# Optimization experiments

Measured on AMD Instinct MI355X. Metric: run time of the kernel, lower is better.

The kernel has to match this reference:

```python
import jax, jax.numpy as jnp
import numpy as np

B, NQ, D, NH, DH = 16, 300, 256, 8, 32
L, P, FFN = 3, 4, 1024
LEVEL_SHAPES = [(80, 80), (40, 40), (20, 20)]
S = sum(h * w for h, w in LEVEL_SHAPES)  # 8400
EPS = 1e-5

PARAM_NAMES = ['wq', 'bq', 'wk', 'bk', 'wv', 'bv', 'wo', 'bo', 'ln1_g', 'ln1_b',
               'w_off', 'b_off', 'w_aw', 'b_aw', 'w_val', 'b_val', 'w_out', 'b_out',
               'ln2_g', 'ln2_b', 'w_fc1', 'b_fc1', 'w_fc2', 'b_fc2', 'ln3_g', 'ln3_b']


def _ln(x, g, b):
    m = jnp.mean(x, -1, keepdims=True)
    v = jnp.mean(jnp.square(x - m), -1, keepdims=True)
    return (x - m) * jax.lax.rsqrt(v + EPS) * g + b


def _bilinear(v_l, loc, Hl, Wl):
    # v_l: [B, Hl*Wl, NH, DH]; loc in [0,1]: [B, NQ, NH, P, 2]
    # matches torch grid_sample(align_corners=False, padding='zeros') with grid=2*loc-1
    x = loc[..., 0] * Wl - 0.5
    y = loc[..., 1] * Hl - 0.5
    x0 = jnp.floor(x)
    y0 = jnp.floor(y)
    vt = v_l.transpose(0, 2, 1, 3)  # [B, NH, Sl, DH]
    out = jnp.zeros((v_l.shape[0], NQ, NH, P, DH), v_l.dtype)
    for dx in (0, 1):
        for dy in (0, 1):
            xi = x0 + dx
            yi = y0 + dy
            w = (1.0 - jnp.abs(x - xi)) * (1.0 - jnp.abs(y - yi))
            valid = (xi >= 0) & (xi < Wl) & (yi >= 0) & (yi < Hl)
            idx = (jnp.clip(yi, 0, Hl - 1) * Wl + jnp.clip(xi, 0, Wl - 1)).astype(jnp.int32)
            idx_t = idx.transpose(0, 2, 1, 3).reshape(idx.shape[0], NH, NQ * P)
            g = jnp.take_along_axis(vt, idx_t[..., None], axis=2)  # [B, NH, NQ*P, DH]
            g = g.reshape(-1, NH, NQ, P, DH).transpose(0, 2, 1, 3, 4)
            out = out + g * (w * valid)[..., None]
    return out  # [B, NQ, NH, P, DH]


def _forward(hidden_states, pos_embed, encoder_hidden_states, reference_points, spatial_shapes, p):
    h = hidden_states
    # ---- self-attention (pos added to q and k only) ----
    hp = h + pos_embed
    q = (hp @ p['wq'] + p['bq']).reshape(B, NQ, NH, DH)
    k = (hp @ p['wk'] + p['bk']).reshape(B, NQ, NH, DH)
    v = (h @ p['wv'] + p['bv']).reshape(B, NQ, NH, DH)
    scores = jnp.einsum('bqhd,bkhd->bhqk', q, k) * (1.0 / np.sqrt(DH).astype(np.float32))
    attn = jax.nn.softmax(scores, -1)
    sa = jnp.einsum('bhqk,bkhd->bqhd', attn, v).reshape(B, NQ, D) @ p['wo'] + p['bo']
    h = _ln(h + sa, p['ln1_g'], p['ln1_b'])

    # ---- multiscale deformable cross-attention ----
    hp = h + pos_embed
    value = (encoder_hidden_states @ p['w_val'] + p['b_val']).reshape(B, S, NH, DH)
    off = (hp @ p['w_off'] + p['b_off']).reshape(B, NQ, NH, L, P, 2)
    aw = jax.nn.softmax((hp @ p['w_aw'] + p['b_aw']).reshape(B, NQ, NH, L * P), -1)
    aw = aw.reshape(B, NQ, NH, L, P)
    normalizer = jnp.stack([spatial_shapes[:, 1], spatial_shapes[:, 0]], -1).astype(h.dtype)  # [L,2] = (W,H)
    loc = reference_points[:, :, None, :, None, :] + off / normalizer[None, None, None, :, None, :]
    out = jnp.zeros((B, NQ, NH, DH), h.dtype)
    start = 0
    for l, (Hl, Wl) in enumerate(LEVEL_SHAPES):
        v_l = value[:, start:start + Hl * Wl]
        sampled = _bilinear(v_l, loc[:, :, :, l], Hl, Wl)  # [B,NQ,NH,P,DH]
        out = out + jnp.sum(sampled * aw[:, :, :, l, :, None], axis=3)
        start += Hl * Wl
    ca = out.reshape(B, NQ, D) @ p['w_out'] + p['b_out']
    h = _ln(h + ca, p['ln2_g'], p['ln2_b'])

    # ---- MLP ----
    mlp = jax.nn.relu(h @ p['w_fc1'] + p['b_fc1']) @ p['w_fc2'] + p['b_fc2']
    return _ln(h + mlp, p['ln3_g'], p['ln3_b'])


def setup_inputs() -> dict:
    key = jax.random.key(0)
    ks = iter(jax.random.split(key, 48))
    def nrm(shape, s=0.02):
        return jax.random.normal(next(ks), shape, jnp.float32) * s
    inp = {
        'hidden_states': jax.random.normal(next(ks), (B, NQ, D), jnp.float32),
        'pos_embed': jax.random.normal(next(ks), (B, NQ, D), jnp.float32),
        'encoder_hidden_states': jax.random.normal(next(ks), (B, S, D), jnp.float32),
        'reference_points': jax.random.uniform(next(ks), (B, NQ, L, 2), jnp.float32),
        'spatial_shapes': jnp.array(LEVEL_SHAPES, jnp.int32),
        'wq': nrm((D, D)), 'bq': jnp.zeros(D),
        'wk': nrm((D, D)), 'bk': jnp.zeros(D),
        'wv': nrm((D, D)), 'bv': jnp.zeros(D),
        'wo': nrm((D, D)), 'bo': jnp.zeros(D),
        'ln1_g': jnp.ones(D), 'ln1_b': jnp.zeros(D),
        'w_off': nrm((D, NH * L * P * 2)), 'b_off': nrm((NH * L * P * 2,), 0.1),
        'w_aw': nrm((D, NH * L * P)), 'b_aw': jnp.zeros(NH * L * P),
        'w_val': nrm((D, D)), 'b_val': jnp.zeros(D),
        'w_out': nrm((D, D)), 'b_out': jnp.zeros(D),
        'ln2_g': jnp.ones(D), 'ln2_b': jnp.zeros(D),
        'w_fc1': nrm((D, FFN)), 'b_fc1': jnp.zeros(FFN),
        'w_fc2': nrm((FFN, D)), 'b_fc2': jnp.zeros(D),
        'ln3_g': jnp.ones(D), 'ln3_b': jnp.zeros(D),
    }
    return inp


def reference(hidden_states, pos_embed, encoder_hidden_states, reference_points, spatial_shapes,
              wq, bq, wk, bk, wv, bv, wo, bo, ln1_g, ln1_b,
              w_off, b_off, w_aw, b_aw, w_val, b_val, w_out, b_out,
              ln2_g, ln2_b, w_fc1, b_fc1, w_fc2, b_fc2, ln3_g, ln3_b):
    p = dict(wq=wq, bq=bq, wk=wk, bk=bk, wv=wv, bv=bv, wo=wo, bo=bo,
             ln1_g=ln1_g, ln1_b=ln1_b, w_off=w_off, b_off=b_off, w_aw=w_aw, b_aw=b_aw,
             w_val=w_val, b_val=b_val, w_out=w_out, b_out=b_out, ln2_g=ln2_g, ln2_b=ln2_b,
             w_fc1=w_fc1, b_fc1=b_fc1, w_fc2=w_fc2, b_fc2=b_fc2, ln3_g=ln3_g, ln3_b=ln3_b)
    return _forward(hidden_states, pos_embed, encoder_hidden_states, reference_points, spatial_shapes, p)
```

## Files before the change

### kernel.cpp

```cpp
#include <hip/hip_runtime.h>
#include <hip/hip_bf16.h>
#include <math.h>

#define B_   16
#define NQ_  300
#define D_   256
#define NH_  8
#define DH_  32
#define L_   3
#define P_   4
#define FFN_ 1024
#define S_   8400
#define ROWS_ (B_*NQ_)
#define NB_   (ROWS_*D_)

typedef __attribute__((ext_vector_type(4))) unsigned short ushort4_t;
typedef __attribute__((ext_vector_type(8))) unsigned short ushort8_t;
typedef __attribute__((ext_vector_type(8))) short bf16x8;
typedef __attribute__((ext_vector_type(4))) float f32x4;

__device__ inline unsigned short f2b(float f) {
    __hip_bfloat16 h = __float2bfloat16(f);
    return __builtin_bit_cast(unsigned short, h);
}
__device__ inline float b2f(unsigned short u) {
    union { unsigned u; float f; } c; c.u = ((unsigned)u) << 16; return c.f;
}

__global__ __launch_bounds__(256) void prep_kernel(
    const float* __restrict__ wq, const float* __restrict__ wk,
    const float* __restrict__ wv, const float* __restrict__ wo,
    const float* __restrict__ w_val, const float* __restrict__ w_out,
    const float* __restrict__ w_off, const float* __restrict__ w_aw,
    const float* __restrict__ w_fc1, const float* __restrict__ w_fc2,
    const float* __restrict__ bq, const float* __restrict__ bk,
    const float* __restrict__ b_off, const float* __restrict__ b_aw,
    unsigned short* __restrict__ wtqk, unsigned short* __restrict__ wtv,
    unsigned short* __restrict__ wto, unsigned short* __restrict__ wtval,
    unsigned short* __restrict__ wtout, unsigned short* __restrict__ wtoa,
    unsigned short* __restrict__ wtfc1, unsigned short* __restrict__ wtfc2,
    float* __restrict__ bqk, float* __restrict__ boa)
{
    const int bid = blockIdx.x;
    if (bid >= 968) {
        int idx = (bid - 968)*256 + threadIdx.x;
        if (idx < 512) bqk[idx] = (idx < 256) ? bq[idx] : bk[idx-256];
        else { int j = idx - 512; if (j < 288) boa[j] = (j < 192) ? b_off[j] : b_aw[j-192]; }
        return;
    }
    const float* src; unsigned short* dst; int K, N, t;
    if      (bid < 64)  { src=wq;    dst=wtqk;         K=256;  N=256;  t=bid; }
    else if (bid < 128) { src=wk;    dst=wtqk+65536;   K=256;  N=256;  t=bid-64; }
    else if (bid < 192) { src=wv;    dst=wtv;          K=256;  N=256;  t=bid-128; }
    else if (bid < 256) { src=wo;    dst=wto;          K=256;  N=256;  t=bid-192; }
    else if (bid < 320) { src=w_val; dst=wtval;        K=256;  N=256;  t=bid-256; }
    else if (bid < 384) { src=w_out; dst=wtout;        K=256;  N=256;  t=bid-320; }
    else if (bid < 432) { src=w_off; dst=wtoa;         K=256;  N=192;  t=bid-384; }
    else if (bid < 456) { src=w_aw;  dst=wtoa+49152;   K=256;  N=96;   t=bid-432; }
    else if (bid < 712) { src=w_fc1; dst=wtfc1;        K=256;  N=1024; t=bid-456; }
    else                { src=w_fc2; dst=wtfc2;        K=1024; N=256;  t=bid-712; }

    __shared__ unsigned short tl[32][33];
    int tid = threadIdx.x;
    int tx = tid & 31, ty = tid >> 5;
    int ntx = N >> 5;
    int n0 = (t % ntx) * 32, k0 = (t / ntx) * 32;
    #pragma unroll
    for (int i = 0; i < 4; ++i)
        tl[tx][ty + i*8] = f2b(src[(size_t)(k0 + ty + i*8)*N + n0 + tx]);
    __syncthreads();
    #pragma unroll
    for (int i = 0; i < 4; ++i)
        dst[(size_t)(n0 + ty + i*8)*K + k0 + tx] = tl[ty + i*8][tx];
}

#define GEMM_PREAMBLE()                                                        \
    const int tid  = threadIdx.x;                                              \
    const int lane = tid & 63;                                                 \
    const int w    = tid >> 6;                                                 \
    const int wr   = w >> 1, wc = w & 1;                                       \
    const int m0   = blockIdx.y * 64;                                          \
    const int n0   = blockIdx.x * 128;                                         \
    const int fr   = lane & 15, fq = lane >> 4;                                \
    const int arow = tid >> 2, aseg = (tid & 3) * 8;                           \
    const int brow = tid >> 1, bseg = (tid & 1) * 16;                          \
    const bool a_ok = (m0 + arow) < M;                                         \
    const bool b_ok = (n0 + brow) < N;                                         \
    const float*          aptr  = A  + (size_t)(m0 + arow)*K + aseg;           \
    const float*          aptr2 = A2 ? A2 + (size_t)(m0 + arow)*K + aseg : (const float*)0; \
    const unsigned short* bptr  = WT + (size_t)(n0 + brow)*K + bseg;           \
    f32x4 acc[2][4];                                                           \
    _Pragma("unroll") for (int m = 0; m < 2; ++m)                              \
        _Pragma("unroll") for (int n = 0; n < 4; ++n)                          \
            acc[m][n] = (f32x4){0.f, 0.f, 0.f, 0.f};                           \
    float4 avA0, avB0, avA1, avB1;                                             \
    ushort8_t bvA0, bvB0, bvA1, bvB1;

#define GEMM_LOAD(avA, avB, bvA, bvB, kk) do {                                 \
    if (a_ok) {                                                                \
        avA = *(const float4*)(aptr + (kk));                                   \
        avB = *(const float4*)(aptr + (kk) + 4);                               \
        if (aptr2) {                                                           \
            float4 x2 = *(const float4*)(aptr2 + (kk));                        \
            float4 y2 = *(const float4*)(aptr2 + (kk) + 4);                    \
            avA.x += x2.x; avA.y += x2.y; avA.z += x2.z; avA.w += x2.w;        \
            avB.x += y2.x; avB.y += y2.y; avB.z += y2.z; avB.w += y2.w;        \
        }                                                                      \
    } else { avA = (float4){0,0,0,0}; avB = (float4){0,0,0,0}; }               \
    if (b_ok) { bvA = *(const ushort8_t*)(bptr + (kk));                        \
                bvB = *(const ushort8_t*)(bptr + (kk) + 8); }                  \
    else { _Pragma("unroll") for (int j = 0; j < 8; ++j){bvA[j]=0;bvB[j]=0;} } \
} while (0)

#define GEMM_STORE_LDS(avA, avB, bvA, bvB) do {                                \
    ushort8_t ac;                                                              \
    ac[0]=f2b(avA.x); ac[1]=f2b(avA.y); ac[2]=f2b(avA.z); ac[3]=f2b(avA.w);    \
    ac[4]=f2b(avB.x); ac[5]=f2b(avB.y); ac[6]=f2b(avB.z); ac[7]=f2b(avB.w);    \
    *(ushort8_t*)&As[arow][aseg]     = ac;                                     \
    *(ushort8_t*)&Bs[brow][bseg]     = bvA;                                    \
    *(ushort8_t*)&Bs[brow][bseg + 8] = bvB;                                    \
} while (0)

#define GEMM_COMPUTE() do {                                                    \
    bf16x8 af[2], bfv[4];                                                      \
    _Pragma("unroll") for (int m = 0; m < 2; ++m)                              \
        af[m] = *(const bf16x8*)&As[wr*32 + m*16 + fr][fq*8];                  \
    _Pragma("unroll") for (int n = 0; n < 4; ++n)                              \
        bfv[n] = *(const bf16x8*)&Bs[wc*64 + n*16 + fr][fq*8];                 \
    _Pragma("unroll") for (int m = 0; m < 2; ++m)                              \
        _Pragma("unroll") for (int n = 0; n < 4; ++n)                          \
            acc[m][n] = __builtin_amdgcn_mfma_f32_16x16x32_bf16(               \
                af[m], bfv[n], acc[m][n], 0, 0, 0);                            \
} while (0)

#define GEMM_KLOOP()                                                           \
    GEMM_LOAD(avA0, avB0, bvA0, bvB0, 0);                                      \
    for (int k0 = 0; k0 < K; k0 += 64) {                                       \
        __syncthreads();                                                       \
        GEMM_STORE_LDS(avA0, avB0, bvA0, bvB0);                                \
        GEMM_LOAD(avA1, avB1, bvA1, bvB1, k0 + 32);                            \
        __syncthreads();                                                       \
        GEMM_COMPUTE();                                                        \
        __syncthreads();                                                       \
        GEMM_STORE_LDS(avA1, avB1, bvA1, bvB1);                                \
        if (k0 + 64 < K) GEMM_LOAD(avA0, avB0, bvA0, bvB0, k0 + 64);           \
        __syncthreads();                                                       \
        GEMM_COMPUTE();                                                        \
    }

__global__ __launch_bounds__(256) void gemm_mfma64(
    const float* __restrict__ A, const float* __restrict__ A2,
    const unsigned short* __restrict__ WT,
    const float* __restrict__ bias, float* __restrict__ C,
    int M, int N, int K, int relu)
{
    __shared__ unsigned short As[64][40];
    __shared__ unsigned short Bs[128][40];
    GEMM_PREAMBLE();
    GEMM_KLOOP();

    #pragma unroll
    for (int n = 0; n < 4; ++n) {
        int col = n0 + wc*64 + n*16 + fr;
        if (col < N) {
            float bcol = bias[col];
            #pragma unroll
            for (int m = 0; m < 2; ++m) {
                int rbase = m0 + wr*32 + m*16 + fq*4;
                #pragma unroll
                for (int r = 0; r < 4; ++r) {
                    int row = rbase + r;
                    if (row < M) {
                        float vv = acc[m][n][r] + bcol;
                        if (relu) vv = fmaxf(vv, 0.f);
                        C[(size_t)row * N + col] = vv;
                    }
                }
            }
        }
    }
}

__global__ __launch_bounds__(256) void stage1_kernel(
    const float* __restrict__ ehs, const float* __restrict__ h_in,
    const float* __restrict__ pos,
    const unsigned short* __restrict__ wtval, const float* __restrict__ b_val,
    unsigned short* __restrict__ val_bf,
    const unsigned short* __restrict__ wtqk, const float* __restrict__ bqk,
    float* __restrict__ buf_qk,
    const unsigned short* __restrict__ wtv, const float* __restrict__ bv,
    float* __restrict__ buf_v)
{
    __shared__ unsigned short As[64][40];
    __shared__ unsigned short Bs[128][40];

    const int bid = blockIdx.x;
    int path, m0, n0, Ncols = 256;
    const float* Ap; const float* A2p = nullptr;
    const unsigned short* Bp; const float* bias; float* C = nullptr;
    if (bid < 4200) {
        path = 0; m0 = (bid >> 1)*64; n0 = (bid & 1)*128;
        Ap = ehs; Bp = wtval; bias = b_val;
    } else if (bid < 4500) {
        int t = bid - 4200;
        path = 1; m0 = (t >> 2)*64; n0 = (t & 3)*128;
        Ap = h_in; A2p = pos; Bp = wtqk; bias = bqk; C = buf_qk; Ncols = 512;
    } else {
        int t = bid - 4500;
        path = 2; m0 = (t >> 1)*64; n0 = (t & 1)*128;
        Ap = h_in; Bp = wtv; bias = bv; C = buf_v;
    }

    const int tid  = threadIdx.x;
    const int lane = tid & 63;
    const int w    = tid >> 6;
    const int wr   = w >> 1, wc = w & 1;
    const int fr   = lane & 15, fq = lane >> 4;
    const int arow = tid >> 2, aseg = (tid & 3) * 8;
    const int brow = tid >> 1, bseg = (tid & 1) * 16;
    const bool a_ok = true, b_ok = true;
    const int K = 256;
    const float*          aptr  = Ap + (size_t)(m0 + arow)*256 + aseg;
    const float*          aptr2 = A2p ? A2p + (size_t)(m0 + arow)*256 + aseg : (const float*)0;
    const unsigned short* bptr  = Bp + (size_t)(n0 + brow)*256 + bseg;

    f32x4 acc[2][4];
    #pragma unroll
    for (int m = 0; m < 2; ++m)
        #pragma unroll
        for (int n = 0; n < 4; ++n)
            acc[m][n] = (f32x4){0.f, 0.f, 0.f, 0.f};
    float4 avA0, avB0, avA1, avB1;
    ushort8_t bvA0, bvB0, bvA1, bvB1;

    GEMM_KLOOP();

    if (path == 0) {
        #pragma unroll
        for (int n = 0; n < 4; ++n) {
            int col = n0 + wc*64 + n*16 + fr;
            int hh = col >> 5, dd = col & 31;
            float bcol = bias[col];
            #pragma unroll
            for (int m = 0; m < 2; ++m) {
                int rbase = m0 + wr*32 + m*16 + fq*4;
                #pragma unroll
                for (int r = 0; r < 4; ++r) {
                    unsigned row = rbase + r;
                    unsigned bb = row / (unsigned)S_;
                    unsigned ss = row - bb * (unsigned)S_;
                    val_bf[((size_t)(bb*NH_ + hh)*S_ + ss)*DH_ + dd] = f2b(acc[m][n][r] + bcol);
                }
            }
        }
    } else {
        #pragma unroll
        for (int n = 0; n < 4; ++n) {
            int col = n0 + wc*64 + n*16 + fr;
            float bcol = bias[col];
            #pragma unroll
            for (int m = 0; m < 2; ++m) {
                int rbase = m0 + wr*32 + m*16 + fq*4;
                #pragma unroll
                for (int r = 0; r < 4; ++r)
                    C[(size_t)(rbase + r) * Ncols + col] = acc[m][n][r] + bcol;
            }
        }
    }
}

__global__ __launch_bounds__(256) void gemm_relu_bf16(
    const float* __restrict__ A, const unsigned short* __restrict__ WT,
    const float* __restrict__ bias, unsigned short* __restrict__ OUT,
    int M, int N, int K)
{
    __shared__ unsigned short As[64][40];
    __shared__ unsigned short Bs[128][40];
    const float* A2 = nullptr;
    GEMM_PREAMBLE();
    GEMM_KLOOP();

    #pragma unroll
    for (int n = 0; n < 4; ++n) {
        int col = n0 + wc*64 + n*16 + fr;
        float bcol = bias[col];
        #pragma unroll
        for (int m = 0; m < 2; ++m) {
            int rbase = m0 + wr*32 + m*16 + fq*4;
            #pragma unroll
            for (int r = 0; r < 4; ++r)
                OUT[(size_t)(rbase + r) * N + col] = f2b(fmaxf(acc[m][n][r] + bcol, 0.f));
        }
    }
}

__global__ __launch_bounds__(256) void gemm_bfA(
    const unsigned short* __restrict__ A, const unsigned short* __restrict__ WT,
    const float* __restrict__ bias, float* __restrict__ C,
    int M, int N, int K)
{
    __shared__ unsigned short As[64][40];
    __shared__ unsigned short Bs[128][40];

    const int tid  = threadIdx.x;
    const int lane = tid & 63;
    const int w    = tid >> 6;
    const int wr   = w >> 1, wc = w & 1;
    const int m0   = blockIdx.y * 64;
    const int n0   = blockIdx.x * 128;
    const int fr   = lane & 15, fq = lane >> 4;
    const int arow = tid >> 2, aseg = (tid & 3) * 8;
    const int brow = tid >> 1, bseg = (tid & 1) * 16;
    const unsigned short* aptr = A  + (size_t)(m0 + arow)*K + aseg;
    const unsigned short* bptr = WT + (size_t)(n0 + brow)*K + bseg;

    f32x4 acc[2][4];
    #pragma unroll
    for (int m = 0; m < 2; ++m)
        #pragma unroll
        for (int n = 0; n < 4; ++n)
            acc[m][n] = (f32x4){0.f, 0.f, 0.f, 0.f};

    ushort8_t au0, au1;
    ushort8_t bvA0, bvB0, bvA1, bvB1;

    au0 = *(const ushort8_t*)(aptr);
    bvA0 = *(const ushort8_t*)(bptr);
    bvB0 = *(const ushort8_t*)(bptr + 8);
    for (int k0 = 0; k0 < K; k0 += 64) {
        __syncthreads();
        *(ushort8_t*)&As[arow][aseg] = au0;
        *(ushort8_t*)&Bs[brow][bseg]     = bvA0;
        *(ushort8_t*)&Bs[brow][bseg + 8] = bvB0;
        au1 = *(const ushort8_t*)(aptr + k0 + 32);
        bvA1 = *(const ushort8_t*)(bptr + k0 + 32);
        bvB1 = *(const ushort8_t*)(bptr + k0 + 40);
        __syncthreads();
        GEMM_COMPUTE();
        __syncthreads();
        *(ushort8_t*)&As[arow][aseg] = au1;
        *(ushort8_t*)&Bs[brow][bseg]     = bvA1;
        *(ushort8_t*)&Bs[brow][bseg + 8] = bvB1;
        if (k0 + 64 < K) {
            au0 = *(const ushort8_t*)(aptr + k0 + 64);
            bvA0 = *(const ushort8_t*)(bptr + k0 + 64);
            bvB0 = *(const ushort8_t*)(bptr + k0 + 72);
        }
        __syncthreads();
        GEMM_COMPUTE();
    }

    #pragma unroll
    for (int n = 0; n < 4; ++n) {
        int col = n0 + wc*64 + n*16 + fr;
        float bcol = bias[col];
        #pragma unroll
        for (int m = 0; m < 2; ++m) {
            int rbase = m0 + wr*32 + m*16 + fq*4;
            #pragma unroll
            for (int r = 0; r < 4; ++r)
                C[(size_t)(rbase + r) * N + col] = acc[m][n][r] + bcol;
        }
    }
}

__global__ __launch_bounds__(256) void self_attn_kernel(
    const float* __restrict__ qk, const float* __restrict__ v,
    float* __restrict__ sa)
{
    __shared__ unsigned short k_sw[304*32];
    __shared__ unsigned short vt[32][312];
    __shared__ unsigned short p_all[4][16][312];

    const int bid  = blockIdx.x;
    const int part = bid % 5;
    const int bh   = bid / 5;
    const int h    = bh & 7;
    const int b    = bh >> 3;
    const int tid  = threadIdx.x;
    const int lane = tid & 63;
    const int w    = tid >> 6;
    const int g    = lane >> 4;
    const int fr   = lane & 15;

    const size_t qbase = (size_t)b*NQ_*512 + h*DH_;
    const size_t kbase = qbase + 256;
    const size_t vbase = (size_t)b*NQ_*D_ + h*DH_;
    const size_t sbase = (size_t)b*NQ_*D_ + h*DH_;

    for (int i = tid; i < 1216; i += 256) {
        int r = i >> 2, u = i & 3;
        ushort8_t kb;
        if (r < NQ_) {
            const float* p8 = qk + kbase + (size_t)r*512 + u*8;
            float4 a0 = *(const float4*)p8;
            float4 a1 = *(const float4*)(p8 + 4);
            kb[0]=f2b(a0.x); kb[1]=f2b(a0.y); kb[2]=f2b(a0.z); kb[3]=f2b(a0.w);
            kb[4]=f2b(a1.x); kb[5]=f2b(a1.y); kb[6]=f2b(a1.z); kb[7]=f2b(a1.w);
        } else {
            #pragma unroll
            for (int j = 0; j < 8; ++j) kb[j] = 0;
        }
        int su = u ^ ((r >> 1) & 3);
        *(ushort8_t*)&k_sw[r*32 + su*8] = kb;
    }
    for (int i = tid; i < 1216; i += 256) {
        int kk = i >> 2, u = i & 3;
        if (kk < NQ_) {
            const float* p8 = v + vbase + (size_t)kk*D_ + u*8;
            float4 a0 = *(const float4*)p8;
            float4 a1 = *(const float4*)(p8 + 4);
            float f[8] = {a0.x,a0.y,a0.z,a0.w,a1.x,a1.y,a1.z,a1.w};
            #pragma unroll
            for (int j = 0; j < 8; ++j) vt[u*8 + j][kk] = f2b(f[j]);
        } else {
            #pragma unroll
            for (int j = 0; j < 8; ++j) vt[u*8 + j][kk] = 0;
        }
    }
    __syncthreads();

    const int q0 = part*64 + w*16;
    const int qi = q0 + fr;
    bf16x8 qf;
    if (qi < NQ_) {
        const float scale = 0.17677669529663687f;
        const float* p8 = qk + qbase + (size_t)qi*512 + g*8;
        float4 a0 = *(const float4*)p8;
        float4 a1 = *(const float4*)(p8 + 4);
        qf[0]=(short)f2b(a0.x*scale); qf[1]=(short)f2b(a0.y*scale);
        qf[2]=(short)f2b(a0.z*scale); qf[3]=(short)f2b(a0.w*scale);
        qf[4]=(short)f2b(a1.x*scale); qf[5]=(short)f2b(a1.y*scale);
        qf[6]=(short)f2b(a1.z*scale); qf[7]=(short)f2b(a1.w*scale);
    } else {
        #pragma unroll
        for (int j = 0; j < 8; ++j) qf[j] = 0;
    }

    const int ksw_u = g ^ ((fr >> 1) & 3);
    f32x4 acc[19];
    #pragma unroll
    for (int t = 0; t < 19; ++t) acc[t] = (f32x4){0.f,0.f,0.f,0.f};
    #pragma unroll
    for (int t = 0; t < 19; ++t) {
        int row = t*16 + fr;
        bf16x8 kf = *(const bf16x8*)&k_sw[row*32 + ksw_u*8];
        acc[t] = __builtin_amdgcn_mfma_f32_16x16x32_bf16(kf, qf, acc[t], 0, 0, 0);
    }
    if (g == 3) acc[18] = (f32x4){-1e30f, -1e30f, -1e30f, -1e30f};

    float m = -1e30f;
    #pragma unroll
    for (int t = 0; t < 19; ++t) {
        #pragma unroll
        for (int r = 0; r < 4; ++r) m = fmaxf(m, acc[t][r]);
    }
    m = fmaxf(m, __shfl_xor(m, 16));
    m = fmaxf(m, __shfl_xor(m, 32));
    float lsum = 0.f;
    #pragma unroll
    for (int t = 0; t < 19; ++t) {
        #pragma unroll
        for (int r = 0; r < 4; ++r) {
            float e = __expf(acc[t][r] - m);
            acc[t][r] = e;
            lsum += e;
        }
    }
    lsum += __shfl_xor(lsum, 16);
    lsum += __shfl_xor(lsum, 32);
    float inv = 1.0f / lsum;

    #pragma unroll
    for (int t = 0; t < 19; ++t) {
        ushort4_t pw = { f2b(acc[t][0]*inv), f2b(acc[t][1]*inv),
                         f2b(acc[t][2]*inv), f2b(acc[t][3]*inv) };
        *(ushort4_t*)&p_all[w][fr][t*16 + g*4] = pw;
    }

    f32x4 o0 = (f32x4){0.f,0.f,0.f,0.f};
    f32x4 o1 = (f32x4){0.f,0.f,0.f,0.f};
    #pragma unroll
    for (int ks = 0; ks < 10; ++ks) {
        int kb = ks*32 + g*8;
        bf16x8 pf, vf0, vf1;
        if (kb < 304) {
            pf  = *(const bf16x8*)&p_all[w][fr][kb];
            vf0 = *(const bf16x8*)&vt[fr][kb];
            vf1 = *(const bf16x8*)&vt[16 + fr][kb];
        } else {
            #pragma unroll
            for (int j = 0; j < 8; ++j) { pf[j] = 0; vf0[j] = 0; vf1[j] = 0; }
        }
        o0 = __builtin_amdgcn_mfma_f32_16x16x32_bf16(pf, vf0, o0, 0, 0, 0);
        o1 = __builtin_amdgcn_mfma_f32_16x16x32_bf16(pf, vf1, o1, 0, 0, 0);
    }

    #pragma unroll
    for (int r = 0; r < 4; ++r) {
        int qo = q0 + g*4 + r;
        if (qo < NQ_) {
            sa[sbase + (size_t)qo*D_ + fr]      = o0[r];
            sa[sbase + (size_t)qo*D_ + 16 + fr] = o1[r];
        }
    }
}

__global__ __launch_bounds__(256) void ln_add_kernel(
    const float* __restrict__ x, const float* __restrict__ y,
    const float* __restrict__ g, const float* __restrict__ bb,
    float* __restrict__ out)
{
    int w = threadIdx.x >> 6, lane = threadIdx.x & 63;
    int row = blockIdx.x*4 + w;
    const float* xr = x + (size_t)row*D_;
    const float* yr = y + (size_t)row*D_;
    float vals[4];
    float s = 0.f;
    #pragma unroll
    for (int i = 0; i < 4; i++) { vals[i] = xr[lane + 64*i] + yr[lane + 64*i]; s += vals[i]; }
    #pragma unroll
    for (int off = 32; off; off >>= 1) s += __shfl_xor(s, off);
    float mean = s * (1.0f/D_);
    float vs = 0.f;
    #pragma unroll
    for (int i = 0; i < 4; i++) { float dd = vals[i]-mean; vs += dd*dd; }
    #pragma unroll
    for (int off = 32; off; off >>= 1) vs += __shfl_xor(vs, off);
    float rstd = rsqrtf(vs*(1.0f/D_) + 1e-5f);
    #pragma unroll
    for (int i = 0; i < 4; i++) {
        int c = lane + 64*i;
        out[(size_t)row*D_ + c] = (vals[i]-mean)*rstd*g[c] + bb[c];
    }
}

__global__ __launch_bounds__(256) void deform_kernel(
    const unsigned short* __restrict__ value, const float* __restrict__ oa,
    const float* __restrict__ refp, float* __restrict__ dout)
{
    int gid = blockIdx.x*256 + threadIdx.x;
    int d = gid & 31;
    int h = (gid >> 5) & 7;
    int bq = gid >> 8;
    int qq = bq % NQ_;
    int b  = bq / NQ_;

    const int starts[3] = {0, 6400, 8000};
    const int Hs[3] = {80, 40, 20};

    const float* offp = oa + (size_t)(b*NQ_+qq)*288 + h*24;
    const float* awp  = oa + (size_t)(b*NQ_+qq)*288 + 192 + h*12;
    const float* refq = refp + (size_t)(b*NQ_+qq)*(L_*2);
    const unsigned short* vb = value + ((size_t)(b*NH_ + h)*S_)*DH_ + d;

    float av[12];
    float mx = -1e30f;
    #pragma unroll
    for (int i = 0; i < 12; ++i) { av[i] = awp[i]; mx = fmaxf(mx, av[i]); }
    float ssum = 0.f;
    #pragma unroll
    for (int i = 0; i < 12; ++i) { av[i] = __expf(av[i]-mx); ssum += av[i]; }
    float sinv = 1.f / ssum;

    float acc = 0.f;
    #pragma unroll
    for (int l = 0; l < L_; l++) {
        int Hl = Hs[l], Wl = Hs[l];
        float rx = refq[l*2+0], ry = refq[l*2+1];
        const unsigned short* vlb = vb + (size_t)starts[l]*DH_;
        #pragma unroll
        for (int p = 0; p < P_; p++) {
            float ox = offp[(l*P_+p)*2+0], oy = offp[(l*P_+p)*2+1];
            float a  = av[l*P_+p] * sinv;
            float x = (rx + ox/(float)Wl)*(float)Wl - 0.5f;
            float y = (ry + oy/(float)Hl)*(float)Hl - 0.5f;
            float x0 = floorf(x), y0 = floorf(y);
            #pragma unroll
            for (int dy = 0; dy < 2; dy++) {
                #pragma unroll
                for (int dx = 0; dx < 2; dx++) {
                    float xi = x0 + dx, yi = y0 + dy;
                    float wgt = (1.f - fabsf(x-xi))*(1.f - fabsf(y-yi));
                    bool valid = (xi >= 0.f) && (xi < (float)Wl) && (yi >= 0.f) && (yi < (float)Hl);
                    if (valid && wgt != 0.f) {
                        int ix = (int)xi, iy = (int)yi;
                        acc += a * wgt * b2f(vlb[(size_t)(iy*Wl + ix)*DH_]);
                    }
                }
            }
        }
    }
    dout[gid] = acc;
}

extern "C" void kernel_launch(void* const* d_in, const int* in_sizes, int n_in,
                              void* d_out, int out_size, void* d_ws, size_t ws_size,
                              hipStream_t stream) {
    (void)in_sizes; (void)n_in; (void)out_size; (void)ws_size;
    const float* h_in  = (const float*)d_in[0];
    const float* pos   = (const float*)d_in[1];
    const float* ehs   = (const float*)d_in[2];
    const float* refp  = (const float*)d_in[3];
    const float* wq    = (const float*)d_in[5];
    const float* bq    = (const float*)d_in[6];
    const float* wk    = (const float*)d_in[7];
    const float* bk    = (const float*)d_in[8];
    const float* wv    = (const float*)d_in[9];
    const float* bv    = (const float*)d_in[10];
    const float* wo    = (const float*)d_in[11];
    const float* bo    = (const float*)d_in[12];
    const float* ln1g  = (const float*)d_in[13];
    const float* ln1b  = (const float*)d_in[14];
    const float* w_off = (const float*)d_in[15];
    const float* b_off = (const float*)d_in[16];
    const float* w_aw  = (const float*)d_in[17];
    const float* b_aw  = (const float*)d_in[18];
    const float* w_val = (const float*)d_in[19];
    const float* b_val = (const float*)d_in[20];
    const float* w_out = (const float*)d_in[21];
    const float* b_out = (const float*)d_in[22];
    const float* ln2g  = (const float*)d_in[23];
    const float* ln2b  = (const float*)d_in[24];
    const float* w_fc1 = (const float*)d_in[25];
    const float* b_fc1 = (const float*)d_in[26];
    const float* w_fc2 = (const float*)d_in[27];
    const float* b_fc2 = (const float*)d_in[28];
    const float* ln3g  = (const float*)d_in[29];
    const float* ln3b  = (const float*)d_in[30];
    float* out = (float*)d_out;

    float* ws = (float*)d_ws;
    float* buf_qk   = ws + 1*(size_t)NB_;
    float* buf_v    = ws + 3*(size_t)NB_;
    float* buf_sa   = ws + 4*(size_t)NB_;
    float* buf_tmp  = ws + 5*(size_t)NB_;
    float* buf_h1   = ws + 6*(size_t)NB_;
    float* buf_h2   = ws + 7*(size_t)NB_;
    float* buf_oa   = ws + 8*(size_t)NB_;
    unsigned short* fc1_bf = (unsigned short*)(ws + 9*(size_t)NB_ + NB_/2);
    unsigned short* val_bf = (unsigned short*)(ws + 13*(size_t)NB_ + NB_/2);

    unsigned short* wtb = (unsigned short*)(ws + 27*(size_t)NB_ + NB_/2);
    unsigned short* wtqk  = wtb;
    unsigned short* wtv   = wtqk  + 131072;
    unsigned short* wto   = wtv   + 65536;
    unsigned short* wtval = wto   + 65536;
    unsigned short* wtout = wtval + 65536;
    unsigned short* wtoa  = wtout + 65536;
    unsigned short* wtfc1 = wtoa  + 73728;
    unsigned short* wtfc2 = wtfc1 + 262144;
    float* bqk = (float*)(wtfc2 + 262144);
    float* boa = bqk + 512;

    dim3 blk(256);

    prep_kernel<<<dim3(972), blk, 0, stream>>>(
        wq, wk, wv, wo, w_val, w_out, w_off, w_aw, w_fc1, w_fc2,
        bq, bk, b_off, b_aw,
        wtqk, wtv, wto, wtval, wtout, wtoa, wtfc1, wtfc2, bqk, boa);

    stage1_kernel<<<dim3(4650), blk, 0, stream>>>(
        ehs, h_in, pos, wtval, b_val, val_bf, wtqk, bqk, buf_qk, wtv, bv, buf_v);

    self_attn_kernel<<<dim3(B_*NH_*5), blk, 0, stream>>>(buf_qk, buf_v, buf_sa);
    gemm_mfma64<<<dim3(2, 75), blk, 0, stream>>>(buf_sa, nullptr, wto, bo, buf_tmp, ROWS_, D_, D_, 0);
    ln_add_kernel<<<dim3(ROWS_/4), blk, 0, stream>>>(h_in, buf_tmp, ln1g, ln1b, buf_h1);
    gemm_mfma64<<<dim3(3, 75), blk, 0, stream>>>(buf_h1, pos, wtoa, boa, buf_oa, ROWS_, 288, D_, 0);
    deform_kernel<<<dim3(NB_/256), blk, 0, stream>>>(val_bf, buf_oa, refp, buf_v);
    gemm_mfma64<<<dim3(2, 75), blk, 0, stream>>>(buf_v, nullptr, wtout, b_out, buf_sa, ROWS_, D_, D_, 0);
    ln_add_kernel<<<dim3(ROWS_/4), blk, 0, stream>>>(buf_h1, buf_sa, ln2g, ln2b, buf_h2);
    gemm_relu_bf16<<<dim3(8, 75), blk, 0, stream>>>(buf_h2, wtfc1, b_fc1, fc1_bf, ROWS_, FFN_, D_);
    gemm_bfA<<<dim3(2, 75), blk, 0, stream>>>(fc1_bf, wtfc2, b_fc2, buf_tmp, ROWS_, D_, FFN_);
    ln_add_kernel<<<dim3(ROWS_/4), blk, 0, stream>>>(buf_h2, buf_tmp, ln3g, ln3b, out);
}
```

Baseline: 230.4 us.

## Fuse residual add and LayerNorm into full-row output GEMM epilogues

Adds GEMM kernels whose 64-row blocks each cover the full 256-column output width. The epilogue adds bias and the residual, reduces row sums and sums of squares across waves through shared memory, and applies LayerNorm directly. This replaces the three separate GEMM + ln_add pairs and removes the intermediate fp32 buffer round trips and three kernel launches. In exchange the grid shrinks to 75 blocks, which lowers parallelism on the GPU, and variance is now computed as E[x²]−mean², which is less numerically stable.

```diff
diff --git a/kernel.cpp b/kernel.cpp
--- a/kernel.cpp
+++ b/kernel.cpp
@@ -294,74 +294,180 @@
     }
 }
 
-__global__ __launch_bounds__(256) void gemm_bfA(
-    const unsigned short* __restrict__ A, const unsigned short* __restrict__ WT,
-    const float* __restrict__ bias, float* __restrict__ C,
-    int M, int N, int K)
+#define GLN_COMPUTE()  do {                                                    \
+    bf16x8 af[2], bfv[8];                                                      \
+    _Pragma("unroll") for (int m = 0; m < 2; ++m)                              \
+        af[m] = *(const bf16x8*)&As[wr*32 + m*16 + fr][fq*8];                  \
+    _Pragma("unroll") for (int n = 0; n < 8; ++n)                              \
+        bfv[n] = *(const bf16x8*)&Bs[wc*128 + n*16 + fr][fq*8];                \
+    _Pragma("unroll") for (int m = 0; m < 2; ++m)                              \
+        _Pragma("unroll") for (int n = 0; n < 8; ++n)                          \
+            acc[m][n] = __builtin_amdgcn_mfma_f32_16x16x32_bf16(               \
+                af[m], bfv[n], acc[m][n], 0, 0, 0);                            \
+} while (0)
+
+#define GLN_EPILOGUE()                                                         \
+    float gcol[8], bcol2[8], biascol[8];                                       \
+    _Pragma("unroll") for (int n = 0; n < 8; ++n) {                            \
+        int col = wc*128 + n*16 + fr;                                          \
+        biascol[n] = bias[col]; gcol[n] = g[col]; bcol2[n] = bb[col];          \
+    }                                                                          \
+    _Pragma("unroll") for (int m = 0; m < 2; ++m) {                            \
+        _Pragma("unroll") for (int r = 0; r < 4; ++r) {                        \
+            int lrow = wr*32 + m*16 + fq*4 + r;                                \
+            float s = 0.f, sq = 0.f;                                           \
+            _Pragma("unroll") for (int n = 0; n < 8; ++n) {                    \
+                float vv = acc[m][n][r] + biascol[n]                           \
+                         + X[(size_t)(m0 + lrow)*256 + wc*128 + n*16 + fr];    \
+                acc[m][n][r] = vv; s += vv; sq += vv*vv;                       \
+            }                                                                  \
+            s  += __shfl_xor(s, 1);  sq += __shfl_xor(sq, 1);                  \
+            s  += __shfl_xor(s, 2);  sq += __shfl_xor(sq, 2);                  \
+            s  += __shfl_xor(s, 4);  sq += __shfl_xor(sq, 4);                  \
+            s  += __shfl_xor(s, 8);  sq += __shfl_xor(sq, 8);                  \
+            if (fr == 0) { psum[lrow][wc] = s; psq[lrow][wc] = sq; }           \
+        }                                                                      \
+    }                                                                          \
+    __syncthreads();                                                           \
+    _Pragma("unroll") for (int m = 0; m < 2; ++m) {                            \
+        _Pragma("unroll") for (int r = 0; r < 4; ++r) {                        \
+            int lrow = wr*32 + m*16 + fq*4 + r;                                \
+            float mean = (psum[lrow][0] + psum[lrow][1]) * (1.0f/256.0f);      \
+            float ex2  = (psq[lrow][0]  + psq[lrow][1])  * (1.0f/256.0f);      \
+            float rstd = rsqrtf(ex2 - mean*mean + 1e-5f);                      \
+            _Pragma("unroll") for (int n = 0; n < 8; ++n) {                    \
+                int col = wc*128 + n*16 + fr;                                  \
+                OUT[(size_t)(m0 + lrow)*256 + col] =                           \
+                    (acc[m][n][r] - mean)*rstd*gcol[n] + bcol2[n];             \
+            }                                                                  \
+        }                                                                      \
+    }
+
+__global__ __launch_bounds__(256) void gemm_ln_f32A(
+    const float* __restrict__ A, const unsigned short* __restrict__ WT,
+    const float* __restrict__ bias, const float* __restrict__ X,
+    const float* __restrict__ g, const float* __restrict__ bb,
+    float* __restrict__ OUT, int K)
 {
     __shared__ unsigned short As[64][40];
-    __shared__ unsigned short Bs[128][40];
+    __shared__ unsigned short Bs[256][40];
+    __shared__ float psum[64][2], psq[64][2];
 
     const int tid  = threadIdx.x;
     const int lane = tid & 63;
     const int w    = tid >> 6;
     const int wr   = w >> 1, wc = w & 1;
-    const int m0   = blockIdx.y * 64;
-    const int n0   = blockIdx.x * 128;
+    const int m0   = blockIdx.x * 64;
     const int fr   = lane & 15, fq = lane >> 4;
     const int arow = tid >> 2, aseg = (tid & 3) * 8;
-    const int brow = tid >> 1, bseg = (tid & 1) * 16;
-    const unsigned short* aptr = A  + (size_t)(m0 + arow)*K + aseg;
-    const unsigned short* bptr = WT + (size_t)(n0 + brow)*K + bseg;
-
-    f32x4 acc[2][4];
+    const float*          aptr = A  + (size_t)(m0 + arow)*K + aseg;
+    const unsigned short* bptr = WT + (size_t)tid*K;
+
+    f32x4 acc[2][8];
     #pragma unroll
     for (int m = 0; m < 2; ++m)
         #pragma unroll
-        for (int n = 0; n < 4; ++n)
+        for (int n = 0; n < 8; ++n)
             acc[m][n] = (f32x4){0.f, 0.f, 0.f, 0.f};
 
-    ushort8_t au0, au1;
-    ushort8_t bvA0, bvB0, bvA1, bvB1;
-
-    au0 = *(const ushort8_t*)(aptr);
-    bvA0 = *(const ushort8_t*)(bptr);
-    bvB0 = *(const ushort8_t*)(bptr + 8);
+    float4 a0x, a0y, a1x, a1y;
+    ushort8_t b0[4], b1[4];
+
+    a0x = *(const float4*)(aptr); a0y = *(const float4*)(aptr + 4);
+    #pragma unroll
+    for (int j = 0; j < 4; ++j) b0[j] = *(const ushort8_t*)(bptr + j*8);
     for (int k0 = 0; k0 < K; k0 += 64) {
         __syncthreads();
-        *(ushort8_t*)&As[arow][aseg] = au0;
-        *(ushort8_t*)&Bs[brow][bseg]     = bvA0;
-        *(ushort8_t*)&Bs[brow][bseg + 8] = bvB0;
-        au1 = *(const ushort8_t*)(aptr + k0 + 32);
-        bvA1 = *(const ushort8_t*)(bptr + k0 + 32);
-        bvB1 = *(const ushort8_t*)(bptr + k0 + 40);
+        {
+            ushort8_t ac;
+            ac[0]=f2b(a0x.x); ac[1]=f2b(a0x.y); ac[2]=f2b(a0x.z); ac[3]=f2b(a0x.w);
+            ac[4]=f2b(a0y.x); ac[5]=f2b(a0y.y); ac[6]=f2b(a0y.z); ac[7]=f2b(a0y.w);
+            *(ushort8_t*)&As[arow][aseg] = ac;
+            #pragma unroll
+            for (int j = 0; j < 4; ++j) *(ushort8_t*)&Bs[tid][j*8] = b0[j];
+        }
+        a1x = *(const float4*)(aptr + k0 + 32); a1y = *(const float4*)(aptr + k0 + 36);
+        #pragma unroll
+        for (int j = 0; j < 4; ++j) b1[j] = *(const ushort8_t*)(bptr + k0 + 32 + j*8);
         __syncthreads();
-        GEMM_COMPUTE();
+        GLN_COMPUTE();
         __syncthreads();
-        *(ushort8_t*)&As[arow][aseg] = au1;
-        *(ushort8_t*)&Bs[brow][bseg]     = bvA1;
-        *(ushort8_t*)&Bs[brow][bseg + 8] = bvB1;
+        {
+            ushort8_t ac;
+            ac[0]=f2b(a1x.x); ac[1]=f2b(a1x.y); ac[2]=f2b(a1x.z); ac[3]=f2b(a1x.w);
+            ac[4]=f2b(a1y.x); ac[5]=f2b(a1y.y); ac[6]=f2b(a1y.z); ac[7]=f2b(a1y.w);
+            *(ushort8_t*)&As[arow][aseg] = ac;
+            #pragma unroll
+            for (int j = 0; j < 4; ++j) *(ushort8_t*)&Bs[tid][j*8] = b1[j];
+        }
         if (k0 + 64 < K) {
-            au0 = *(const ushort8_t*)(aptr + k0 + 64);
-            bvA0 = *(const ushort8_t*)(bptr + k0 + 64);
-            bvB0 = *(const ushort8_t*)(bptr + k0 + 72);
+            a0x = *(const float4*)(aptr + k0 + 64); a0y = *(const float4*)(aptr + k0 + 68);
+            #pragma unroll
+            for (int j = 0; j < 4; ++j) b0[j] = *(const ushort8_t*)(bptr + k0 + 64 + j*8);
         }
         __syncthreads();
-        GEMM_COMPUTE();
-    }
-
-    #pragma unroll
-    for (int n = 0; n < 4; ++n) {
-        int col = n0 + wc*64 + n*16 + fr;
-        float bcol = bias[col];
-        #pragma unroll
-        for (int m = 0; m < 2; ++m) {
-            int rbase = m0 + wr*32 + m*16 + fq*4;
-            #pragma unroll
-            for (int r = 0; r < 4; ++r)
-                C[(size_t)(rbase + r) * N + col] = acc[m][n][r] + bcol;
-        }
-    }
+        GLN_COMPUTE();
+    }
+
+    GLN_EPILOGUE();
+}
+
+__global__ __launch_bounds__(256) void gemm_ln_bf16A(
+    const unsigned short* __restrict__ A, const unsigned short* __restrict__ WT,
+    const float* __restrict__ bias, const float* __restrict__ X,
+    const float* __restrict__ g, const float* __restrict__ bb,
+    float* __restrict__ OUT, int K)
+{
+    __shared__ unsigned short As[64][40];
+    __shared__ unsigned short Bs[256][40];
+    __shared__ float psum[64][2], psq[64][2];
+
+    const int tid  = threadIdx.x;
+    const int lane = tid & 63;
+    const int w    = tid >> 6;
+    const int wr   = w >> 1, wc = w & 1;
+    const int m0   = blockIdx.x * 64;
+    const int fr   = lane & 15, fq = lane >> 4;
+    const int arow = tid >> 2, aseg = (tid & 3) * 8;
+    const unsigned short* aptr = A  + (size_t)(m0 + arow)*K + aseg;
+    const unsigned short* bptr = WT + (size_t)tid*K;
+
+    f32x4 acc[2][8];
+    #pragma unroll
+    for (int m = 0; m < 2; ++m)
+        #pragma unroll
+        for (int n = 0; n < 8; ++n)
+            acc[m][n] = (f32x4){0.f, 0.f, 0.f, 0.f};
+
+    ushort8_t a0, a1, b0[4], b1[4];
+
+    a0 = *(const ushort8_t*)(aptr);
+    #pragma unroll
+    for (int j = 0; j < 4; ++j) b0[j] = *(const ushort8_t*)(bptr + j*8);
+    for (int k0 = 0; k0 < K; k0 += 64) {
+        __syncthreads();
+        *(ushort8_t*)&As[arow][aseg] = a0;
+        #pragma unroll
+        for (int j = 0; j < 4; ++j) *(ushort8_t*)&Bs[tid][j*8] = b0[j];
+        a1 = *(const ushort8_t*)(aptr + k0 + 32);
+        #pragma unroll
+        for (int j = 0; j < 4; ++j) b1[j] = *(const ushort8_t*)(bptr + k0 + 32 + j*8);
+        __syncthreads();
+        GLN_COMPUTE();
+        __syncthreads();
+        *(ushort8_t*)&As[arow][aseg] = a1;
+        #pragma unroll
+        for (int j = 0; j < 4; ++j) *(ushort8_t*)&Bs[tid][j*8] = b1[j];
+        if (k0 + 64 < K) {
+            a0 = *(const ushort8_t*)(aptr + k0 + 64);
+            #pragma unroll
+            for (int j = 0; j < 4; ++j) b0[j] = *(const ushort8_t*)(bptr + k0 + 64 + j*8);
+        }
+        __syncthreads();
+        GLN_COMPUTE();
+    }
+
+    GLN_EPILOGUE();
 }
 
 __global__ __launch_bounds__(256) void self_attn_kernel(
@@ -503,35 +609,6 @@
             sa[sbase + (size_t)qo*D_ + fr]      = o0[r];
             sa[sbase + (size_t)qo*D_ + 16 + fr] = o1[r];
         }
-    }
-}
-
-__global__ __launch_bounds__(256) void ln_add_kernel(
-    const float* __restrict__ x, const float* __restrict__ y,
-    const float* __restrict__ g, const float* __restrict__ bb,
-    float* __restrict__ out)
-{
-    int w = threadIdx.x >> 6, lane = threadIdx.x & 63;
-    int row = blockIdx.x*4 + w;
-    const float* xr = x + (size_t)row*D_;
-    const float* yr = y + (size_t)row*D_;
-    float vals[4];
-    float s = 0.f;
-    #pragma unroll
-    for (int i = 0; i < 4; i++) { vals[i] = xr[lane + 64*i] + yr[lane + 64*i]; s += vals[i]; }
-    #pragma unroll
-    for (int off = 32; off; off >>= 1) s += __shfl_xor(s, off);
-    float mean = s * (1.0f/D_);
-    float vs = 0.f;
-    #pragma unroll
-    for (int i = 0; i < 4; i++) { float dd = vals[i]-mean; vs += dd*dd; }
-    #pragma unroll
-    for (int off = 32; off; off >>= 1) vs += __shfl_xor(vs, off);
-    float rstd = rsqrtf(vs*(1.0f/D_) + 1e-5f);
-    #pragma unroll
-    for (int i = 0; i < 4; i++) {
-        int c = lane + 64*i;
-        out[(size_t)row*D_ + c] = (vals[i]-mean)*rstd*g[c] + bb[c];
     }
 }
 
@@ -634,7 +711,6 @@
     float* buf_qk   = ws + 1*(size_t)NB_;
     float* buf_v    = ws + 3*(size_t)NB_;
     float* buf_sa   = ws + 4*(size_t)NB_;
-    float* buf_tmp  = ws + 5*(size_t)NB_;
     float* buf_h1   = ws + 6*(size_t)NB_;
     float* buf_h2   = ws + 7*(size_t)NB_;
     float* buf_oa   = ws + 8*(size_t)NB_;
@@ -664,13 +740,13 @@
         ehs, h_in, pos, wtval, b_val, val_bf, wtqk, bqk, buf_qk, wtv, bv, buf_v);
 
     self_attn_kernel<<<dim3(B_*NH_*5), blk, 0, stream>>>(buf_qk, buf_v, buf_sa);
-    gemm_mfma64<<<dim3(2, 75), blk, 0, stream>>>(buf_sa, nullptr, wto, bo, buf_tmp, ROWS_, D_, D_, 0);
-    ln_add_kernel<<<dim3(ROWS_/4), blk, 0, stream>>>(h_in, buf_tmp, ln1g, ln1b, buf_h1);
+    gemm_ln_f32A<<<dim3(ROWS_/64), blk, 0, stream>>>(
+        buf_sa, wto, bo, h_in, ln1g, ln1b, buf_h1, 256);
     gemm_mfma64<<<dim3(3, 75), blk, 0, stream>>>(buf_h1, pos, wtoa, boa, buf_oa, ROWS_, 288, D_, 0);
     deform_kernel<<<dim3(NB_/256), blk, 0, stream>>>(val_bf, buf_oa, refp, buf_v);
-    gemm_mfma64<<<dim3(2, 75), blk, 0, stream>>>(buf_v, nullptr, wtout, b_out, buf_sa, ROWS_, D_, D_, 0);
-    ln_add_kernel<<<dim3(ROWS_/4), blk, 0, stream>>>(buf_h1, buf_sa, ln2g, ln2b, buf_h2);
+    gemm_ln_f32A<<<dim3(ROWS_/64), blk, 0, stream>>>(
+        buf_v, wtout, b_out, buf_h1, ln2g, ln2b, buf_h2, 256);
     gemm_relu_bf16<<<dim3(8, 75), blk, 0, stream>>>(buf_h2, wtfc1, b_fc1, fc1_bf, ROWS_, FFN_, D_);
-    gemm_bfA<<<dim3(2, 75), blk, 0, stream>>>(fc1_bf, wtfc2, b_fc2, buf_tmp, ROWS_, D_, FFN_);
-    ln_add_kernel<<<dim3(ROWS_/4), blk, 0, stream>>>(buf_h2, buf_tmp, ln3g, ln3b, out);
-}
+    gemm_ln_bf16A<<<dim3(ROWS_/64), blk, 0, stream>>>(
+        fc1_bf, wtfc2, b_fc2, buf_h2, ln3g, ln3b, out, FFN_);
+}
```

After: 231.1 us. About the same (+0.3%).
